# Kernel optimization log

Measured on AMD Instinct MI355X. Metric: run time of the kernel, lower is better.

## Reference

```python
import jax, jax.numpy as jnp
from jax import lax
import numpy as np

B, T, I, H, O = 256, 1024, 64, 256, 1


def setup_inputs() -> dict:
    key = jax.random.key(0)
    ks = jax.random.split(key, 7)
    s = 0.05
    return {
        "x": jax.random.normal(ks[0], (B, T, I), dtype=jnp.float32),
        "W_ih": jax.random.normal(ks[1], (4 * H, I), dtype=jnp.float32) * s,
        "W_hh": jax.random.normal(ks[2], (4 * H, H), dtype=jnp.float32) * s,
        "b_ih": jax.random.normal(ks[3], (4 * H,), dtype=jnp.float32) * s,
        "b_hh": jax.random.normal(ks[4], (4 * H,), dtype=jnp.float32) * s,
        "fc_w": jax.random.normal(ks[5], (O, H), dtype=jnp.float32) * s,
        "fc_b": jax.random.normal(ks[6], (O,), dtype=jnp.float32) * s,
    }


def _lstm_last_hidden(x, W_ih, W_hh, b_ih, b_hh):
    # x: [B, T, I] -> last hidden state h_T: [B, H]
    h_dim = W_hh.shape[1]
    xT = jnp.swapaxes(x, 0, 1)                      # [T, B, I]
    # Precompute input contribution to gates for all timesteps (one big GEMM)
    x_gates = jnp.einsum("tbi,gi->tbg", xT, W_ih) + b_ih + b_hh  # [T, B, 4H]

    def step(carry, xg):
        h, c = carry
        g = xg + h @ W_hh.T                         # [B, 4H]
        i, f, gg, o = jnp.split(g, 4, axis=-1)       # torch gate order i,f,g,o
        i = jax.nn.sigmoid(i)
        f = jax.nn.sigmoid(f)
        gg = jnp.tanh(gg)
        o = jax.nn.sigmoid(o)
        c = f * c + i * gg
        h = o * jnp.tanh(c)
        return (h, c), None

    b = x.shape[0]
    h0 = jnp.zeros((b, h_dim), dtype=x.dtype)
    c0 = jnp.zeros((b, h_dim), dtype=x.dtype)
    (h_last, _), _ = lax.scan(step, (h0, c0), x_gates)
    return h_last


def reference(x, W_ih, W_hh, b_ih, b_hh, fc_w, fc_b):
    h_last = _lstm_last_hidden(x, W_ih, W_hh, b_ih, b_hh)  # [B, H]
    return h_last @ fc_w.T + fc_b                           # [B, O]
```

## Files before the change

kernel.cpp:

```cpp
#include <hip/hip_runtime.h>
#include <stdint.h>


#define T_ 1024
#define I_ 64
#define H_ 256
#define NQUAD 4
#define NGROUP 32
#define MB 8
#define QH 64
#define HROW 272

#define UNITS_PER_GROUP 1024
#define UNITS_PER_PARITY (NGROUP * UNITS_PER_GROUP)
#define SENT_CAP (1 << 16)

typedef float floatx4 __attribute__((ext_vector_type(4)));
typedef __bf16 bf16x8 __attribute__((ext_vector_type(8)));
typedef unsigned short ushortx8 __attribute__((ext_vector_type(8)));
typedef unsigned int uint32;
typedef unsigned long long u64;

__device__ __forceinline__ float bf2f(uint32 u16) {
  uint32 u = u16 << 16;
  return __builtin_bit_cast(float, u);
}
__device__ __forceinline__ bf16x8 packbf8(floatx4 a, floatx4 b) {
  bf16x8 r;
  r[0] = (__bf16)a[0]; r[1] = (__bf16)a[1];
  r[2] = (__bf16)a[2]; r[3] = (__bf16)a[3];
  r[4] = (__bf16)b[0]; r[5] = (__bf16)b[1];
  r[6] = (__bf16)b[2]; r[7] = (__bf16)b[3];
  return r;
}
__device__ __forceinline__ float fast_sig(float v) {
  return 1.0f / (1.0f + __expf(-v));
}
__device__ __forceinline__ float fast_tanh(float v) {
  float e = __expf(2.0f * v);
  return 1.0f - 2.0f / (e + 1.0f);
}
__device__ __forceinline__ u64 aload64(const u64* p) {
  return __hip_atomic_load(p, __ATOMIC_RELAXED, __HIP_MEMORY_SCOPE_AGENT);
}

__global__ __launch_bounds__(512, 1) void lstm_main(
    const float* __restrict__ x, const float* __restrict__ W_ih,
    const float* __restrict__ W_hh, const float* __restrict__ b_ih,
    const float* __restrict__ b_hh, u64* __restrict__ units) {
  const int tid = threadIdx.x;
  const int bid = blockIdx.x;
  const int q = bid >> 5;
  const int g = bid & 31;
  const int w8 = tid >> 6;
  const int gate = w8 & 3;
  const int ss = w8 >> 2;
  const int lane = tid & 63;
  const int ln = lane & 15;
  const int lk = lane >> 4;

  __shared__ float xch[4][2][2][16][8];
  __shared__ __align__(16) unsigned short h_lds[MB][HROW];
  unsigned short* const hflat = &h_lds[0][0];

  const size_t gbase = (size_t)g * UNITS_PER_GROUP;

  {
    uint32* p = (uint32*)hflat;
    for (int i = tid; i < MB * HROW / 2; i += 512) p[i] = 0u;
  }

  bf16x8 wf[2][10];
  float bias[2];
#pragma unroll
  for (int j = 0; j < 2; ++j) {
    const int row = gate * 256 + q * QH + ss * 32 + j * 16 + ln;
    bias[j] = b_ih[row] + b_hh[row];
#pragma unroll
    for (int kc = 0; kc < 10; ++kc) {
      const int kk = kc * 32 + lk * 8;
      const float* src = (kk < I_) ? (W_ih + (size_t)row * I_ + kk)
                                   : (W_hh + (size_t)row * H_ + (kk - I_));
      floatx4 f0 = *(const floatx4*)src;
      floatx4 f1 = *(const floatx4*)(src + 4);
      wf[j][kc] = packbf8(f0, f1);
    }
  }

  const bool two = (tid < 256);
  const int k0 = tid >> 8;
  const int qq0 = k0 + (k0 >= q ? 1 : 0);
  const int idx0 = tid & 255;
  const int qq1 = 2 + (2 >= q ? 1 : 0);
  const int idx1 = tid;
  const size_t uoff0 = gbase + (size_t)(qq0 * 256 + idx0);
  const size_t uoff1 = gbase + (size_t)(qq1 * 256 + idx1);
  const int ldsoff0 = (idx0 >> 5) * HROW + qq0 * QH + (idx0 & 31) * 2;
  const int ldsoff1 = (idx1 >> 5) * HROW + qq1 * QH + (idx1 & 31) * 2;

  const int mb = ln & 7;
  const float* xrow = x + ((size_t)(g * MB + mb)) * T_ * I_;
  const int um = tid >> 6;
  const int uhl = tid & 63;
  const int ssu = uhl >> 5, u5 = uhl & 31;
  const int uj = u5 >> 4, un = u5 & 15;
  float c_reg = 0.0f;

  __syncthreads();

#pragma unroll 1
  for (int t = 0; t < T_; ++t) {
    floatx4 xf0, xf1, xf2, xf3;
    {
      const float* src = xrow + t * I_ + lk * 8;
      xf0 = *(const floatx4*)(src);
      xf1 = *(const floatx4*)(src + 4);
      xf2 = *(const floatx4*)(src + 32);
      xf3 = *(const floatx4*)(src + 36);
    }

    if (t > 0) {
      const u64* up0 = units + (size_t)(t & 1) * UNITS_PER_PARITY + uoff0;
      const u64* up1 = units + (size_t)(t & 1) * UNITS_PER_PARITY + uoff1;
      u64 v0 = aload64(up0);
      u64 v1 = 0;
      if (two) v1 = aload64(up1);
      bool ok = ((uint32)(v0 >> 32) == (uint32)t);
      if (two) ok &= ((uint32)(v1 >> 32) == (uint32)t);
      int it = 0;
      while (!__all(ok) && ++it < SENT_CAP) {
        u64 n0 = 0, n1 = 0;
        if (!ok) {
          n0 = aload64(up0);
          if (two) n1 = aload64(up1);
        }
        __builtin_amdgcn_s_sleep(1);
        if (!ok) {
          v0 = n0; v1 = n1;
          ok = ((uint32)(v0 >> 32) == (uint32)t);
          if (two) ok &= ((uint32)(v1 >> 32) == (uint32)t);
        }
      }
      *(uint32*)&hflat[ldsoff0] = (uint32)v0;
      if (two) *(uint32*)&hflat[ldsoff1] = (uint32)v1;
    }
    __syncthreads();

    bf16x8 af[10];
    af[0] = packbf8(xf0, xf1);
    af[1] = packbf8(xf2, xf3);
    const unsigned short* hrow = &h_lds[mb][0];
#pragma unroll
    for (int kc = 2; kc < 10; ++kc) {
      af[kc] =
          __builtin_bit_cast(bf16x8, *(const ushortx8*)(hrow + (kc - 2) * 32 +
                                                        lk * 8));
    }

    floatx4 acc[2];
    acc[0] = (floatx4){bias[0], bias[0], bias[0], bias[0]};
    acc[1] = (floatx4){bias[1], bias[1], bias[1], bias[1]};
#pragma unroll
    for (int kc = 0; kc < 10; ++kc) {
      acc[0] = __builtin_amdgcn_mfma_f32_16x16x32_bf16(af[kc], wf[0][kc],
                                                       acc[0], 0, 0, 0);
      acc[1] = __builtin_amdgcn_mfma_f32_16x16x32_bf16(af[kc], wf[1][kc],
                                                       acc[1], 0, 0, 0);
    }

#pragma unroll
    for (int j = 0; j < 2; ++j) {
      floatx4 v = acc[j];
      if (gate == 2) {
        v[0] = fast_tanh(v[0]); v[1] = fast_tanh(v[1]);
        v[2] = fast_tanh(v[2]); v[3] = fast_tanh(v[3]);
      } else {
        v[0] = fast_sig(v[0]); v[1] = fast_sig(v[1]);
        v[2] = fast_sig(v[2]); v[3] = fast_sig(v[3]);
      }
      if (lk < 2) {
        *(floatx4*)&xch[gate][ss][j][ln][lk * 4] = v;
      }
    }
    __syncthreads();

    float ig = xch[0][ssu][uj][un][um];
    float fg = xch[1][ssu][uj][un][um];
    float gg = xch[2][ssu][uj][un][um];
    float og = xch[3][ssu][uj][un][um];
    c_reg = fg * c_reg + ig * gg;
    float hv = og * fast_tanh(c_reg);

    unsigned short hb = __builtin_bit_cast(unsigned short, (__bf16)hv);
    int pv = __shfl_xor((int)hb, 1);
    if ((tid & 1) == 0) {
      uint32 dword = (uint32)hb | ((uint32)(unsigned short)pv << 16);
      *(uint32*)&hflat[um * HROW + q * QH + uhl] = dword;
      u64 val = (u64)dword | ((u64)(uint32)(t + 1) << 32);
      const size_t uoff = gbase + (size_t)(q * 256 + um * 32 + (uhl >> 1));
      if (t == T_ - 1) {
        __hip_atomic_store(units + 2 * (size_t)UNITS_PER_PARITY + uoff, val,
                           __ATOMIC_RELAXED, __HIP_MEMORY_SCOPE_AGENT);
      } else {
        __hip_atomic_store(units + (size_t)((t + 1) & 1) * UNITS_PER_PARITY +
                               uoff,
                           val, __ATOMIC_RELAXED, __HIP_MEMORY_SCOPE_AGENT);
      }
    }
  }
}

__global__ void lstm_fc(const u64* __restrict__ units,
                        const float* __restrict__ fc_w,
                        const float* __restrict__ fc_b,
                        float* __restrict__ out) {
  const int b = threadIdx.x;
  const int g = b >> 3, m = b & 7;
  const u64* base =
      units + 2 * (size_t)UNITS_PER_PARITY + (size_t)g * UNITS_PER_GROUP;
  float sum = fc_b[0];
#pragma unroll 8
  for (int u = 0; u < 128; ++u) {
    const int qq = u >> 5, p = u & 31;
    u64 v = aload64(base + qq * 256 + m * 32 + p);
    uint32 lo = (uint32)v;
    const int d = qq * QH + 2 * p;
    sum += bf2f(lo & 0xffffu) * fc_w[d] + bf2f(lo >> 16) * fc_w[d + 1];
  }
  out[b] = sum;
}

extern "C" void kernel_launch(void* const* d_in, const int* in_sizes, int n_in,
                              void* d_out, int out_size, void* d_ws,
                              size_t ws_size, hipStream_t stream) {
  const float* x    = (const float*)d_in[0];
  const float* W_ih = (const float*)d_in[1];
  const float* W_hh = (const float*)d_in[2];
  const float* b_ih = (const float*)d_in[3];
  const float* b_hh = (const float*)d_in[4];
  const float* fc_w = (const float*)d_in[5];
  const float* fc_b = (const float*)d_in[6];
  float* out = (float*)d_out;

  u64* units = (u64*)d_ws;

  lstm_main<<<dim3(NGROUP * NQUAD), dim3(512), 0, stream>>>(
      x, W_ih, W_hh, b_ih, b_hh, units);
  lstm_fc<<<dim3(1), dim3(256), 0, stream>>>(units, fc_w, fc_b, out);
}
```

Measured before the change: 2.748 ms.

## Split LSTM hidden dim across two blocks with all gates per wave

Each batch group is now handled by 2 blocks, each owning half the hidden units, instead of 4 quarter-blocks. Every wave now computes all four gates for its 16 hidden columns. The gate nonlinearities and the cell update therefore stay in registers, which removes the LDS gate-exchange buffer and one __syncthreads per timestep. The h buffer in LDS is double-buffered by timestep parity, and each block polls only its partner's half. The cost is twice the weight registers per thread (wf[4][10]), a longer serial MFMA chain per wave, and half as many blocks in total.

After: 3.120 ms. +13.6%, slower.

```diff
diff --git a/kernel.cpp b/kernel.cpp
--- a/kernel.cpp
+++ b/kernel.cpp
@@ -5,11 +5,10 @@
 #define T_ 1024
 #define I_ 64
 #define H_ 256
-#define NQUAD 4
 #define NGROUP 32
 #define MB 8
-#define QH 64
-#define HROW 272
+#define HH 128
+#define HROW 264
 
 #define UNITS_PER_GROUP 1024
 #define UNITS_PER_PARITY (NGROUP * UNITS_PER_GROUP)
@@ -43,38 +42,39 @@
 __device__ __forceinline__ u64 aload64(const u64* p) {
   return __hip_atomic_load(p, __ATOMIC_RELAXED, __HIP_MEMORY_SCOPE_AGENT);
 }
-
-__global__ __launch_bounds__(512, 1) void lstm_main(
+__device__ __forceinline__ void astore64(u64* p, u64 v) {
+  __hip_atomic_store(p, v, __ATOMIC_RELAXED, __HIP_MEMORY_SCOPE_AGENT);
+}
+
+__global__ __launch_bounds__(512, 2) void lstm_main(
     const float* __restrict__ x, const float* __restrict__ W_ih,
     const float* __restrict__ W_hh, const float* __restrict__ b_ih,
     const float* __restrict__ b_hh, u64* __restrict__ units) {
   const int tid = threadIdx.x;
   const int bid = blockIdx.x;
-  const int q = bid >> 5;
+  const int half = bid >> 5;
   const int g = bid & 31;
-  const int w8 = tid >> 6;
-  const int gate = w8 & 3;
-  const int ss = w8 >> 2;
+  const int wv = tid >> 6;
   const int lane = tid & 63;
   const int ln = lane & 15;
   const int lk = lane >> 4;
 
-  __shared__ float xch[4][2][2][16][8];
-  __shared__ __align__(16) unsigned short h_lds[MB][HROW];
-  unsigned short* const hflat = &h_lds[0][0];
+  __shared__ __align__(16) unsigned short h_lds[2][MB][HROW];
 
   const size_t gbase = (size_t)g * UNITS_PER_GROUP;
+  const size_t obase = gbase + (size_t)half * 512;
+  const size_t pbase = gbase + (size_t)(half ^ 1) * 512;
 
   {
-    uint32* p = (uint32*)hflat;
-    for (int i = tid; i < MB * HROW / 2; i += 512) p[i] = 0u;
-  }
-
-  bf16x8 wf[2][10];
-  float bias[2];
-#pragma unroll
-  for (int j = 0; j < 2; ++j) {
-    const int row = gate * 256 + q * QH + ss * 32 + j * 16 + ln;
+    uint32* p = (uint32*)&h_lds[0][0][0];
+    for (int i = tid; i < 2 * MB * HROW / 2; i += 512) p[i] = 0u;
+  }
+
+  bf16x8 wf[4][10];
+  float bias[4];
+#pragma unroll
+  for (int j = 0; j < 4; ++j) {
+    const int row = j * 256 + half * HH + wv * 16 + ln;
     bias[j] = b_ih[row] + b_hh[row];
 #pragma unroll
     for (int kc = 0; kc < 10; ++kc) {
@@ -87,24 +87,14 @@
     }
   }
 
-  const bool two = (tid < 256);
-  const int k0 = tid >> 8;
-  const int qq0 = k0 + (k0 >= q ? 1 : 0);
-  const int idx0 = tid & 255;
-  const int qq1 = 2 + (2 >= q ? 1 : 0);
-  const int idx1 = tid;
-  const size_t uoff0 = gbase + (size_t)(qq0 * 256 + idx0);
-  const size_t uoff1 = gbase + (size_t)(qq1 * 256 + idx1);
-  const int ldsoff0 = (idx0 >> 5) * HROW + qq0 * QH + (idx0 & 31) * 2;
-  const int ldsoff1 = (idx1 >> 5) * HROW + qq1 * QH + (idx1 & 31) * 2;
-
   const int mb = ln & 7;
   const float* xrow = x + ((size_t)(g * MB + mb)) * T_ * I_;
-  const int um = tid >> 6;
-  const int uhl = tid & 63;
-  const int ssu = uhl >> 5, u5 = uhl & 31;
-  const int uj = u5 >> 4, un = u5 & 15;
-  float c_reg = 0.0f;
+  const int pm = tid >> 6;
+  const int pcol = (half ^ 1) * HH + 2 * (tid & 63);
+  const int ppair = wv * 8 + (ln >> 1);
+  const int ocol = half * HH + wv * 16 + ln;
+
+  floatx4 c_reg = (floatx4){0.f, 0.f, 0.f, 0.f};
 
   __syncthreads();
 
@@ -120,91 +110,73 @@
     }
 
     if (t > 0) {
-      const u64* up0 = units + (size_t)(t & 1) * UNITS_PER_PARITY + uoff0;
-      const u64* up1 = units + (size_t)(t & 1) * UNITS_PER_PARITY + uoff1;
-      u64 v0 = aload64(up0);
-      u64 v1 = 0;
-      if (two) v1 = aload64(up1);
-      bool ok = ((uint32)(v0 >> 32) == (uint32)t);
-      if (two) ok &= ((uint32)(v1 >> 32) == (uint32)t);
+      u64* up = units + (size_t)(t & 1) * UNITS_PER_PARITY + pbase + tid;
+      u64 v = aload64(up);
+      bool ok = ((uint32)(v >> 32) == (uint32)t);
       int it = 0;
       while (!__all(ok) && ++it < SENT_CAP) {
-        u64 n0 = 0, n1 = 0;
-        if (!ok) {
-          n0 = aload64(up0);
-          if (two) n1 = aload64(up1);
-        }
+        u64 n = 0;
+        if (!ok) n = aload64(up);
         __builtin_amdgcn_s_sleep(1);
         if (!ok) {
-          v0 = n0; v1 = n1;
-          ok = ((uint32)(v0 >> 32) == (uint32)t);
-          if (two) ok &= ((uint32)(v1 >> 32) == (uint32)t);
+          v = n;
+          ok = ((uint32)(v >> 32) == (uint32)t);
         }
       }
-      *(uint32*)&hflat[ldsoff0] = (uint32)v0;
-      if (two) *(uint32*)&hflat[ldsoff1] = (uint32)v1;
+      *(uint32*)&h_lds[t & 1][pm][pcol] = (uint32)v;
     }
     __syncthreads();
 
-    bf16x8 af[10];
-    af[0] = packbf8(xf0, xf1);
-    af[1] = packbf8(xf2, xf3);
-    const unsigned short* hrow = &h_lds[mb][0];
-#pragma unroll
-    for (int kc = 2; kc < 10; ++kc) {
-      af[kc] =
-          __builtin_bit_cast(bf16x8, *(const ushortx8*)(hrow + (kc - 2) * 32 +
-                                                        lk * 8));
-    }
-
-    floatx4 acc[2];
-    acc[0] = (floatx4){bias[0], bias[0], bias[0], bias[0]};
-    acc[1] = (floatx4){bias[1], bias[1], bias[1], bias[1]};
+    bf16x8 a0 = packbf8(xf0, xf1);
+    bf16x8 a1 = packbf8(xf2, xf3);
+    const unsigned short* hrow = &h_lds[t & 1][mb][0];
+
+    floatx4 acc[4];
+#pragma unroll
+    for (int j = 0; j < 4; ++j)
+      acc[j] = (floatx4){bias[j], bias[j], bias[j], bias[j]};
 #pragma unroll
     for (int kc = 0; kc < 10; ++kc) {
-      acc[0] = __builtin_amdgcn_mfma_f32_16x16x32_bf16(af[kc], wf[0][kc],
-                                                       acc[0], 0, 0, 0);
-      acc[1] = __builtin_amdgcn_mfma_f32_16x16x32_bf16(af[kc], wf[1][kc],
-                                                       acc[1], 0, 0, 0);
-    }
-
-#pragma unroll
-    for (int j = 0; j < 2; ++j) {
-      floatx4 v = acc[j];
-      if (gate == 2) {
-        v[0] = fast_tanh(v[0]); v[1] = fast_tanh(v[1]);
-        v[2] = fast_tanh(v[2]); v[3] = fast_tanh(v[3]);
-      } else {
-        v[0] = fast_sig(v[0]); v[1] = fast_sig(v[1]);
-        v[2] = fast_sig(v[2]); v[3] = fast_sig(v[3]);
+      bf16x8 a;
+      if (kc == 0) a = a0;
+      else if (kc == 1) a = a1;
+      else
+        a = __builtin_bit_cast(
+            bf16x8, *(const ushortx8*)(hrow + (kc - 2) * 32 + lk * 8));
+#pragma unroll
+      for (int j = 0; j < 4; ++j)
+        acc[j] = __builtin_amdgcn_mfma_f32_16x16x32_bf16(a, wf[j][kc],
+                                                         acc[j], 0, 0, 0);
+    }
+
+    if (lk < 2) {
+      floatx4 iv, fv, gv, ov;
+#pragma unroll
+      for (int r = 0; r < 4; ++r) {
+        iv[r] = fast_sig(acc[0][r]);
+        fv[r] = fast_sig(acc[1][r]);
+        gv[r] = fast_tanh(acc[2][r]);
+        ov[r] = fast_sig(acc[3][r]);
       }
-      if (lk < 2) {
-        *(floatx4*)&xch[gate][ss][j][ln][lk * 4] = v;
-      }
-    }
-    __syncthreads();
-
-    float ig = xch[0][ssu][uj][un][um];
-    float fg = xch[1][ssu][uj][un][um];
-    float gg = xch[2][ssu][uj][un][um];
-    float og = xch[3][ssu][uj][un][um];
-    c_reg = fg * c_reg + ig * gg;
-    float hv = og * fast_tanh(c_reg);
-
-    unsigned short hb = __builtin_bit_cast(unsigned short, (__bf16)hv);
-    int pv = __shfl_xor((int)hb, 1);
-    if ((tid & 1) == 0) {
-      uint32 dword = (uint32)hb | ((uint32)(unsigned short)pv << 16);
-      *(uint32*)&hflat[um * HROW + q * QH + uhl] = dword;
-      u64 val = (u64)dword | ((u64)(uint32)(t + 1) << 32);
-      const size_t uoff = gbase + (size_t)(q * 256 + um * 32 + (uhl >> 1));
-      if (t == T_ - 1) {
-        __hip_atomic_store(units + 2 * (size_t)UNITS_PER_PARITY + uoff, val,
-                           __ATOMIC_RELAXED, __HIP_MEMORY_SCOPE_AGENT);
-      } else {
-        __hip_atomic_store(units + (size_t)((t + 1) & 1) * UNITS_PER_PARITY +
-                               uoff,
-                           val, __ATOMIC_RELAXED, __HIP_MEMORY_SCOPE_AGENT);
+      c_reg = fv * c_reg + iv * gv;
+#pragma unroll
+      for (int r = 0; r < 4; ++r) {
+        float hv = ov[r] * fast_tanh(c_reg[r]);
+        unsigned short hb = __builtin_bit_cast(unsigned short, (__bf16)hv);
+        int pv = __shfl_xor((int)hb, 1);
+        if ((ln & 1) == 0) {
+          const int m = lk * 4 + r;
+          uint32 dword = (uint32)hb | ((uint32)(unsigned short)pv << 16);
+          u64 val = (u64)dword | ((u64)(uint32)(t + 1) << 32);
+          const size_t uoff = obase + (size_t)m * 64 + ppair;
+          if (t == T_ - 1) {
+            astore64(units + 2 * (size_t)UNITS_PER_PARITY + uoff, val);
+          } else {
+            astore64(units + (size_t)((t + 1) & 1) * UNITS_PER_PARITY + uoff,
+                     val);
+            *(uint32*)&h_lds[(t + 1) & 1][m][ocol] = dword;
+          }
+        }
       }
     }
   }
@@ -219,12 +191,12 @@
   const u64* base =
       units + 2 * (size_t)UNITS_PER_PARITY + (size_t)g * UNITS_PER_GROUP;
   float sum = fc_b[0];
-#pragma unroll 8
+#pragma unroll 4
   for (int u = 0; u < 128; ++u) {
-    const int qq = u >> 5, p = u & 31;
-    u64 v = aload64(base + qq * 256 + m * 32 + p);
+    const int hf = u >> 6, pair = u & 63;
+    u64 v = aload64(base + hf * 512 + m * 64 + pair);
     uint32 lo = (uint32)v;
-    const int d = qq * QH + 2 * p;
+    const int d = hf * HH + 2 * pair;
     sum += bf2f(lo & 0xffffu) * fc_w[d] + bf2f(lo >> 16) * fc_w[d + 1];
   }
   out[b] = sum;
@@ -244,7 +216,7 @@
 
   u64* units = (u64*)d_ws;
 
-  lstm_main<<<dim3(NGROUP * NQUAD), dim3(512), 0, stream>>>(
+  lstm_main<<<dim3(NGROUP * 2), dim3(512), 0, stream>>>(
       x, W_ih, W_hh, b_ih, b_hh, units);
   lstm_fc<<<dim3(1), dim3(256), 0, stream>>>(units, fc_w, fc_b, out);
 }
```
